# Optimization experiments

Measured on AMD Instinct MI355X. Metric: run time of the kernel, lower is better.

The kernel has to match this reference:

```python
import jax, jax.numpy as jnp
import numpy as np

LN_EPS = 1e-5
NEG_SLOPE = 0.01  # torch F.leaky_relu default


def setup_inputs() -> dict:
    key = jax.random.key(0)
    ks = jax.random.split(key, 12)
    B, N, Do, Na = 128, 32, 128, 16
    H, Dk, Dv = 4, 64, 64
    Dio = Do + Na  # 144
    g = lambda k, shape, fan_in: jax.random.normal(k, shape, jnp.float32) / np.sqrt(fan_in)
    return {
        "states": jax.random.normal(ks[0], (B, N, Do), jnp.float32),
        "policies": jax.random.uniform(ks[1], (B, N, Na), jnp.float32),
        "actions": jax.random.uniform(ks[2], (B, N, Na), jnp.float32),
        "W_se": g(ks[3], (Do, 128), Do),
        "b_se": jnp.zeros((128,), jnp.float32),
        "W_sape": g(ks[4], (Dio, 128), Dio),
        "b_sape": jnp.zeros((128,), jnp.float32),
        "Wk": g(ks[5], (H, 128, Dk), 128),
        "Wq": g(ks[6], (H, 128, Dk), 128),
        "Wv": g(ks[7], (H, 128, Dv), 128),
        "ln_g": jnp.ones((H, Dv), jnp.float32),
        "ln_b": jnp.zeros((H, Dv), jnp.float32),
        "W_f1": g(ks[8], (H * Dv, 64), H * Dv),
        "W_f2": g(ks[9], (64, 1), 64),
    }


def _layernorm(x, g, b):
    mu = x.mean(-1, keepdims=True)
    var = ((x - mu) ** 2).mean(-1, keepdims=True)
    return (x - mu) * jax.lax.rsqrt(var + LN_EPS) * g + b


def reference(states, policies, actions, W_se, b_se, W_sape, b_sape,
              Wk, Wq, Wv, ln_g, ln_b, W_f1, W_f2):
    leaky = lambda x: jax.nn.leaky_relu(x, NEG_SLOPE)
    B, N, _ = states.shape
    H, _, Dv = Wv.shape
    d_k = Wk.shape[-1]

    se = leaky(states @ W_se + b_se)  # [B,N,128]

    oa = jnp.concatenate([states, actions], axis=-1)   # [B,N,Dio]
    op = jnp.concatenate([states, policies], axis=-1)  # [B,N,Dio]
    # oap[b,j,k] = op[b,k] if j==k else oa[b,k]  (place_policies/place_actions masks)
    eye = jnp.eye(N, dtype=states.dtype)[None, :, :, None]  # [1,N,N,1]
    oap = eye * op[:, None, :, :] + (1.0 - eye) * oa[:, None, :, :]  # [B,N,N,Dio]
    x = leaky(oap @ W_sape + b_sape)  # [B,N,N,128]

    key = jnp.einsum('bnd,hde->bhne', se, Wk)  # [B,H,N,Dk]
    qry = jnp.einsum('bnd,hde->bhne', se, Wq)
    scores = jnp.einsum('bhie,bhke->bhik', qry, key) / jnp.sqrt(jnp.asarray(d_k, states.dtype))
    w = jax.nn.softmax(scores, axis=-1)  # [B,H,N,N]

    av = jnp.einsum('bjkd,hde->bhjke', x, Wv)  # [B,H,N,N,Dv]
    # node_features[b,h,i,j] = sum_k w[b,h,i,k] * av[b,h,j,k]  (fuses torch's O(N^3) repeat)
    nf = jnp.einsum('bhik,bhjke->bhije', w, av)  # [B,H,N,N,Dv]
    nf = _layernorm(nf, ln_g[None, :, None, None, :], ln_b[None, :, None, None, :])

    mh = jnp.moveaxis(nf, 1, 3).reshape(B, N, N, H * Dv)  # concat heads on last dim
    value = leaky(mh @ W_f1) @ W_f2  # [B,N,N,1]
    return value, w
```

## Files before the change

kernel.cpp:

```cpp
#include <hip/hip_runtime.h>
#include <hip/hip_bf16.h>

#define B 128
#define N 32
#define DO 128
#define NA 16
#define H 4
#define DK 64
#define DV 64
#define LN_EPS 1e-5f
#define NEG_SLOPE 0.01f

typedef unsigned short u16;
typedef __attribute__((ext_vector_type(8))) short bf16x8;
typedef __attribute__((ext_vector_type(4))) float f32x4;

__device__ __forceinline__ float leaky(float x) {
    return x >= 0.f ? x : NEG_SLOPE * x;
}

__device__ __forceinline__ u16 f2bf(float x) {
    union { float f; unsigned int u; } v; v.f = x;
    unsigned int r = (v.u + 0x7FFF + ((v.u >> 16) & 1)) >> 16;
    return (u16)r;
}

__device__ __forceinline__ float bf2f(u16 x) {
    union { unsigned int u; float f; } v; v.u = ((unsigned int)x) << 16;
    return v.f;
}

template<int CTRL>
__device__ __forceinline__ float dppadd(float x) {
    return x + __int_as_float(__builtin_amdgcn_update_dpp(
        0, __float_as_int(x), CTRL, 0xF, 0xF, true));
}

__global__ __launch_bounds__(256) void kP(
    const float* __restrict__ Wk, const float* __restrict__ Wq,
    const float* __restrict__ Wv, const float* __restrict__ W_se,
    const float* __restrict__ W_sape, const float* __restrict__ ln_g,
    const float* __restrict__ ln_b, const float* __restrict__ W_f1,
    u16* __restrict__ wTb, u16* __restrict__ wseT, u16* __restrict__ wsapeT,
    u16* __restrict__ sapeTail, u16* __restrict__ wTg,
    float* __restrict__ GW, float* __restrict__ BW)
{
    const int blk = blockIdx.x;
    const int t   = threadIdx.x;
    __shared__ float wls[8192];

    if (blk < 4) {
        const int hh = blk;
        for (int m = 0; m < 3; m++) {
            const float* src = (m == 0 ? Wq : (m == 1 ? Wk : Wv)) + hh * 8192;
            for (int idx = t; idx < 2048; idx += 256)
                ((float4*)wls)[idx] = ((const float4*)src)[idx];
            __syncthreads();
            u16* dst = wTb + (hh * 3 + m) * 8192;
            for (int idx = t; idx < 8192; idx += 256) {
                const int n = idx >> 7, k = idx & 127;
                dst[idx] = f2bf(wls[k * 64 + n]);
            }
            __syncthreads();
        }
    } else if (blk == 4 || blk == 5) {
        const float* src = (blk == 4) ? W_se : W_sape;
        u16* dst = (blk == 4) ? wseT : wsapeT;
        for (int chunk = 0; chunk < 2; chunk++) {
            const int k0 = chunk * 64;
            for (int idx = t; idx < 2048; idx += 256)
                ((float4*)wls)[idx] = ((const float4*)(src + k0 * 128))[idx];
            __syncthreads();
            for (int idx = t; idx < 8192; idx += 256) {
                const int n = idx >> 6, kk = idx & 63;
                dst[n * 128 + k0 + kk] = f2bf(wls[kk * 128 + n]);
            }
            __syncthreads();
        }
        if (blk == 5) {
            for (int idx = t; idx < 2048; idx += 256)
                wls[idx] = W_sape[128 * 128 + idx];
            __syncthreads();
            for (int idx = t; idx < 4096; idx += 256) {
                const int n = idx >> 5, kk = idx & 31;
                sapeTail[n * 32 + kk] = (kk < 16) ? f2bf(wls[kk * 128 + n]) : (u16)0;
            }
        }
    } else {
        for (int idx = t; idx < 16384; idx += 256) {
            const int hh = idx >> 12, c = (idx >> 6) & 63, ee = idx & 63;
            wTg[idx] = f2bf(ln_g[hh * 64 + ee] * W_f1[(hh * 64 + ee) * 64 + c]);
        }
        {
            const int hh = t >> 6, c = t & 63;
            float g = 0.f;
            #pragma unroll 4
            for (int ee = 0; ee < 64; ee++)
                g += ln_g[hh * 64 + ee] * W_f1[(hh * 64 + ee) * 64 + c];
            GW[t] = g;
        }
        {
            const int c = t & 63, qq = t >> 6;
            float bacc = 0.f;
            #pragma unroll 4
            for (int r = 0; r < 64; r++)
                bacc += ln_b[qq * 64 + r] * W_f1[(qq * 64 + r) * 64 + c];
            wls[qq * 64 + c] = bacc;
        }
        __syncthreads();
        if (t < 64) BW[t] = wls[t] + wls[64 + t] + wls[128 + t] + wls[192 + t];
    }
}

__global__ __launch_bounds__(1024, 8) void kB(
    const float* __restrict__ states, const float* __restrict__ actions,
    const float* __restrict__ policies,
    const float* __restrict__ b_se, const float* __restrict__ b_sape,
    const u16* __restrict__ wTb, const u16* __restrict__ wseT,
    const u16* __restrict__ wsapeT, const u16* __restrict__ sapeTail,
    const u16* __restrict__ wTg,
    float* __restrict__ w_out,
    float* __restrict__ SG, float* __restrict__ DG,
    float* __restrict__ sumS, float* __restrict__ sumS2,
    float* __restrict__ sumD, float* __restrict__ sumD2,
    float* __restrict__ dotSD)
{
    const int bh   = blockIdx.x;
    const int b    = bh >> 2;
    const int h    = bh & 3;
    const int t    = threadIdx.x;
    const int wave = t >> 6;
    const int e    = t & 63;
    const int q16  = e >> 4;
    const int l16  = e & 15;

    __shared__ alignas(16) u16   sST[32 * 136];
    __shared__ alignas(16) u16   actA[32 * 40];
    __shared__ alignas(16) u16   polA[32 * 40];
    __shared__ alignas(16) u16   sSE[32 * 136];
    __shared__ alignas(16) u16   sXA[32 * 136];
    __shared__ alignas(16) u16   sXP[32 * 136];
    __shared__ alignas(16) u16   qb[32 * 72];
    __shared__ alignas(16) u16   kb[32 * 72];
    __shared__ alignas(16) u16   avaT[64 * 40];
    __shared__ alignas(16) u16   diffb[32 * 72];
    __shared__ alignas(16) u16   wb[32 * 40];
    __shared__ alignas(16) float S32[32 * 68];
    __shared__ alignas(16) u16   Sb[32 * 72];

    const int mtP   = wave >> 3, ntP = wave & 7;
    const int bcolP = ntP * 16 + l16;
    bf16x8 pse[4];
    {
        const u16* bse_p = wseT + bcolP * 128;
        #pragma unroll
        for (int ks = 0; ks < 4; ks++)
            pse[ks] = *(const bf16x8*)&bse_p[ks * 32 + q16 * 8];
    }
    const bf16x8 btP   = *(const bf16x8*)&sapeTail[bcolP * 32 + q16 * 8];
    const float  bse_c = b_se[bcolP];
    const float  bsp_c = b_sape[bcolP];

    {
        const int r = t >> 5, c4 = (t & 31) * 4;
        const float4 s4 = *(const float4*)&states[(b * 32 + r) * 128 + c4];
        ushort4 u;
        u.x = f2bf(s4.x); u.y = f2bf(s4.y); u.z = f2bf(s4.z); u.w = f2bf(s4.w);
        *(ushort4*)&sST[r * 136 + c4] = u;
    }
    if (t < 512) {
        const int r = t >> 4, c = t & 15;
        actA[r * 40 + c]      = f2bf(actions[(b * 32 + r) * 16 + c]);
        actA[r * 40 + 16 + c] = 0;
    } else {
        const int t2 = t - 512, r = t2 >> 4, c = t2 & 15;
        polA[r * 40 + c]      = f2bf(policies[(b * 32 + r) * 16 + c]);
        polA[r * 40 + 16 + c] = 0;
    }

    bf16x8 psp[4];
    {
        const u16* bsp_p = wsapeT + bcolP * 128;
        #pragma unroll
        for (int ks = 0; ks < 4; ks++)
            psp[ks] = *(const bf16x8*)&bsp_p[ks * 32 + q16 * 8];
    }
    __syncthreads();

    f32x4 acc[2];
    bf16x8 pw0[4];
    {
        const int mt = mtP, nt = ntP;
        const int arow = mt * 16 + l16;
        const int bcol = bcolP;
        f32x4 a_se = {0.f,0.f,0.f,0.f}, a_sp = {0.f,0.f,0.f,0.f};
        f32x4 a_oa = {0.f,0.f,0.f,0.f}, a_op = {0.f,0.f,0.f,0.f};
        #pragma unroll
        for (int ks = 0; ks < 4; ks++) {
            const bf16x8 af = *(const bf16x8*)&sST[arow * 136 + ks * 32 + q16 * 8];
            a_se = __builtin_amdgcn_mfma_f32_16x16x32_bf16(af, pse[ks], a_se, 0, 0, 0);
            a_sp = __builtin_amdgcn_mfma_f32_16x16x32_bf16(af, psp[ks], a_sp, 0, 0, 0);
        }
        a_oa = __builtin_amdgcn_mfma_f32_16x16x32_bf16(
            *(const bf16x8*)&actA[arow * 40 + q16 * 8], btP, a_oa, 0, 0, 0);
        a_op = __builtin_amdgcn_mfma_f32_16x16x32_bf16(
            *(const bf16x8*)&polA[arow * 40 + q16 * 8], btP, a_op, 0, 0, 0);

        {
            const int tau0 = wave * 2;
            const int mat0 = tau0 >> 3;
            const int widx0 = (mat0 == 0) ? 0 : (mat0 == 1 ? 1 : 2);
            const int nt0 = tau0 & 3;
            const u16* wsrc0 = wTb + ((h * 3 + widx0) * 64 + nt0 * 16 + l16) * 128;
            #pragma unroll
            for (int ks = 0; ks < 4; ks++)
                pw0[ks] = *(const bf16x8*)&wsrc0[ks * 32 + q16 * 8];
        }

        const int r0 = mt * 16 + q16 * 4;
        #pragma unroll
        for (int v = 0; v < 4; v++) {
            sSE[(r0 + v) * 136 + bcol] = f2bf(leaky(a_se[v] + bse_c));
            sXA[(r0 + v) * 136 + bcol] = f2bf(leaky(a_sp[v] + a_oa[v] + bsp_c));
            sXP[(r0 + v) * 136 + bcol] = f2bf(leaky(a_sp[v] + a_op[v] + bsp_c));
        }
    }
    __syncthreads();

    #pragma unroll
    for (int p = 0; p < 2; p++) {
        const int tau = wave * 2 + p;
        const int mat = tau >> 3;
        const int mt  = (tau >> 2) & 1, nt = tau & 3;
        const u16* X  = (mat <= 1) ? sSE : (mat == 2 ? sXA : sXP);
        const int widx = (mat == 0) ? 0 : (mat == 1 ? 1 : 2);
        const int arow = mt * 16 + l16;
        const u16* wsrc = wTb + ((h * 3 + widx) * 64 + nt * 16 + l16) * 128;
        f32x4 a = {0.f, 0.f, 0.f, 0.f};
        #pragma unroll
        for (int ks = 0; ks < 4; ks++) {
            const bf16x8 af = *(const bf16x8*)&X[arow * 136 + ks * 32 + q16 * 8];
            const bf16x8 bf = (p == 0) ? pw0[ks]
                                       : *(const bf16x8*)&wsrc[ks * 32 + q16 * 8];
            a = __builtin_amdgcn_mfma_f32_16x16x32_bf16(af, bf, a, 0, 0, 0);
        }
        acc[p] = a;
    }
    #pragma unroll
    for (int p = 0; p < 2; p++) {
        const int tau = wave * 2 + p;
        const int mat = tau >> 3;
        const int mt  = (tau >> 2) & 1, nt = tau & 3;
        const int c   = nt * 16 + l16;
        const int r0  = mt * 16 + q16 * 4;
        if (mat == 0) {
            #pragma unroll
            for (int v = 0; v < 4; v++) qb[(r0 + v) * 72 + c] = f2bf(acc[p][v]);
        } else if (mat == 1) {
            #pragma unroll
            for (int v = 0; v < 4; v++) kb[(r0 + v) * 72 + c] = f2bf(acc[p][v]);
        } else if (mat == 2) {
            #pragma unroll
            for (int v = 0; v < 4; v++) avaT[c * 40 + (r0 + v)] = f2bf(acc[p][v]);
        }
    }
    __syncthreads();

    bf16x8 pwg[2];
    if (wave >= 8) {
        const int nt = (wave - 8) & 3;
        const u16* wgp = wTg + (h * 64 + nt * 16 + l16) * 64;
        #pragma unroll
        for (int ks = 0; ks < 2; ks++)
            pwg[ks] = *(const bf16x8*)&wgp[ks * 32 + q16 * 8];
    }
    if (wave < 2) {
        const int mt = wave;
        f32x4 s0 = {0.f,0.f,0.f,0.f}, s1 = {0.f,0.f,0.f,0.f};
        #pragma unroll
        for (int ks = 0; ks < 2; ks++) {
            const bf16x8 af = *(const bf16x8*)&qb[(mt * 16 + l16) * 72 + ks * 32 + q16 * 8];
            const bf16x8 b0 = *(const bf16x8*)&kb[l16 * 72 + ks * 32 + q16 * 8];
            const bf16x8 b1 = *(const bf16x8*)&kb[(16 + l16) * 72 + ks * 32 + q16 * 8];
            s0 = __builtin_amdgcn_mfma_f32_16x16x32_bf16(af, b0, s0, 0, 0, 0);
            s1 = __builtin_amdgcn_mfma_f32_16x16x32_bf16(af, b1, s1, 0, 0, 0);
        }
        #pragma unroll
        for (int v = 0; v < 4; v++) {
            float a0 = s0[v] * 0.125f, a1 = s1[v] * 0.125f;
            float mx = fmaxf(a0, a1);
            #pragma unroll
            for (int m = 1; m < 16; m <<= 1) mx = fmaxf(mx, __shfl_xor(mx, m));
            float e0 = __expf(a0 - mx), e1 = __expf(a1 - mx);
            float sm = e0 + e1;
            #pragma unroll
            for (int m = 1; m < 16; m <<= 1) sm += __shfl_xor(sm, m);
            const float inv = 1.f / sm;
            e0 *= inv; e1 *= inv;
            const int i = mt * 16 + q16 * 4 + v;
            wb[i * 40 + l16]      = f2bf(e0);
            wb[i * 40 + 16 + l16] = f2bf(e1);
            w_out[(bh * 32 + i) * 32 + l16]      = e0;
            w_out[(bh * 32 + i) * 32 + 16 + l16] = e1;
        }
    } else if (wave >= 12) {
        #pragma unroll
        for (int p = 0; p < 2; p++) {
            const int tau = wave * 2 + p;
            const int mt  = (tau >> 2) & 1, nt = tau & 3;
            const int c   = nt * 16 + l16;
            const int r0  = mt * 16 + q16 * 4;
            #pragma unroll
            for (int v = 0; v < 4; v++) {
                const float av = bf2f(avaT[c * 40 + (r0 + v)]);
                diffb[(r0 + v) * 72 + c] = f2bf(acc[p][v] - av);
            }
        }
    }
    __syncthreads();

    if (wave < 8) {
        const int mt = wave >> 2, nt = wave & 3;
        const bf16x8 af = *(const bf16x8*)&wb[(mt * 16 + l16) * 40 + q16 * 8];
        const bf16x8 bf = *(const bf16x8*)&avaT[(nt * 16 + l16) * 40 + q16 * 8];
        f32x4 a = {0.f, 0.f, 0.f, 0.f};
        a = __builtin_amdgcn_mfma_f32_16x16x32_bf16(af, bf, a, 0, 0, 0);
        const int c = nt * 16 + l16, r0 = mt * 16 + q16 * 4;
        #pragma unroll
        for (int v = 0; v < 4; v++) {
            S32[(r0 + v) * 68 + c] = a[v];
            Sb[(r0 + v) * 72 + c]  = f2bf(a[v]);
        }
    } else {
        const int w8 = wave - 8;
        const int mt = w8 >> 2, nt = w8 & 3;
        f32x4 a = {0.f, 0.f, 0.f, 0.f};
        #pragma unroll
        for (int ks = 0; ks < 2; ks++) {
            const bf16x8 af = *(const bf16x8*)&diffb[(mt * 16 + l16) * 72 + ks * 32 + q16 * 8];
            a = __builtin_amdgcn_mfma_f32_16x16x32_bf16(af, pwg[ks], a, 0, 0, 0);
        }
        const int c = nt * 16 + l16, r0 = mt * 16 + q16 * 4;
        #pragma unroll
        for (int v = 0; v < 4; v++)
            DG[(bh * 32 + r0 + v) * 64 + c] = a[v];
    }
    if (t < 32) {
        float s1 = 0.f, s2 = 0.f;
        #pragma unroll
        for (int e8 = 0; e8 < 8; e8++) {
            const uint4 u = *(const uint4*)&diffb[t * 72 + e8 * 8];
            const unsigned int uu[4] = {u.x, u.y, u.z, u.w};
            #pragma unroll
            for (int q = 0; q < 4; q++) {
                const float fl = __uint_as_float(uu[q] << 16);
                const float fh = __uint_as_float(uu[q] & 0xffff0000u);
                s1 += fl + fh;
                s2 += fl * fl + fh * fh;
            }
        }
        sumD[bh * 32 + t] = s1; sumD2[bh * 32 + t] = s2;
    }
    __syncthreads();

    if (wave < 4) {
        const int mt = wave >> 1, nt = wave & 1;
        f32x4 a = {0.f, 0.f, 0.f, 0.f};
        #pragma unroll
        for (int ks = 0; ks < 2; ks++) {
            const bf16x8 af = *(const bf16x8*)&Sb[(mt * 16 + l16) * 72 + ks * 32 + q16 * 8];
            const bf16x8 bf = *(const bf16x8*)&diffb[(nt * 16 + l16) * 72 + ks * 32 + q16 * 8];
            a = __builtin_amdgcn_mfma_f32_16x16x32_bf16(af, bf, a, 0, 0, 0);
        }
        const int j = nt * 16 + l16, r0 = mt * 16 + q16 * 4;
        #pragma unroll
        for (int v = 0; v < 4; v++)
            dotSD[(bh * 32 + r0 + v) * 32 + j] = a[v];
    } else if (wave >= 8) {
        const int w8 = wave - 8;
        const int mt = w8 >> 2, nt = w8 & 3;
        f32x4 a = {0.f, 0.f, 0.f, 0.f};
        #pragma unroll
        for (int ks = 0; ks < 2; ks++) {
            const bf16x8 af = *(const bf16x8*)&Sb[(mt * 16 + l16) * 72 + ks * 32 + q16 * 8];
            a = __builtin_amdgcn_mfma_f32_16x16x32_bf16(af, pwg[ks], a, 0, 0, 0);
        }
        const int c = nt * 16 + l16, r0 = mt * 16 + q16 * 4;
        #pragma unroll
        for (int v = 0; v < 4; v++)
            SG[(bh * 32 + r0 + v) * 64 + c] = a[v];
    } else if (t >= 256 && t < 288) {
        const int r = t - 256;
        float s1 = 0.f, s2 = 0.f;
        #pragma unroll
        for (int e4 = 0; e4 < 16; e4++) {
            const float4 v4 = *(const float4*)&S32[r * 68 + e4 * 4];
            s1 += v4.x + v4.y + v4.z + v4.w;
            s2 += v4.x * v4.x + v4.y * v4.y + v4.z * v4.z + v4.w * v4.w;
        }
        sumS[bh * 32 + r] = s1; sumS2[bh * 32 + r] = s2;
    }
}

__global__ __launch_bounds__(256) void kC(
    const float* __restrict__ SG, const float* __restrict__ DG,
    const float* __restrict__ sumS, const float* __restrict__ sumS2,
    const float* __restrict__ sumD, const float* __restrict__ sumD2,
    const float* __restrict__ dotSD, const float* __restrict__ w_all,
    const float* __restrict__ GW, const float* __restrict__ BW,
    const float* __restrict__ W_f2, float* __restrict__ value)
{
    const int blk = blockIdx.x;
    const int b   = blk >> 3;
    const int i0  = ((blk >> 1) & 3) * 8;
    const int j0  = (blk & 1) * 16;
    const int t   = threadIdx.x;
    const int w0  = t >> 6;
    const int e   = t & 63;

    __shared__ alignas(16) float pk[8 * 16 * 12];

    for (int idx = t; idx < 512; idx += 256) {
        const int ii = idx >> 6, jl = (idx >> 2) & 15, hh = idx & 3;
        const int j  = j0 + jl;
        const int hi = (b * 4 + hh) * 32 + i0 + ii;
        const int hj = (b * 4 + hh) * 32 + j;
        const float wv  = w_all[hi * 32 + j];
        const float dsd = dotSD[hi * 32 + j];
        const float mu  = (sumS[hi] + wv * sumD[hj]) * (1.f / 64.f);
        const float e2  = (sumS2[hi] + 2.f * wv * dsd + wv * wv * sumD2[hj]) * (1.f / 64.f);
        const float var = fmaxf(e2 - mu * mu, 0.f);
        const float inv = rsqrtf(var + LN_EPS);
        float* rec = &pk[(ii * 16 + jl) * 12 + hh * 3];
        rec[0] = inv;
        rec[1] = inv * wv;
        rec[2] = -inv * mu;
    }

    const float bwr = BW[e];
    const float f2v = W_f2[e];
    float gw[4], sg[8][4];
    #pragma unroll
    for (int hh = 0; hh < 4; hh++) {
        gw[hh] = GW[hh * 64 + e];
        #pragma unroll
        for (int ii = 0; ii < 8; ii++)
            sg[ii][hh] = SG[((b * 4 + hh) * 32 + i0 + ii) * 64 + e];
    }
    __syncthreads();

    for (int jb = 0; jb < 4; jb++) {
        const int jl = jb * 4 + w0;
        const int j  = j0 + jl;
        float d[4];
        #pragma unroll
        for (int hh = 0; hh < 4; hh++)
            d[hh] = DG[((b * 4 + hh) * 32 + j) * 64 + e];
        #pragma unroll
        for (int ii = 0; ii < 8; ii++) {
            const float* rec = &pk[(ii * 16 + jl) * 12];
            const f32x4 r0 = *(const f32x4*)rec;
            const f32x4 r1 = *(const f32x4*)(rec + 4);
            const f32x4 r2 = *(const f32x4*)(rec + 8);
            float z = bwr;
            z += r0[0] * sg[ii][0]; z += r0[1] * d[0]; z += r0[2] * gw[0];
            z += r0[3] * sg[ii][1]; z += r1[0] * d[1]; z += r1[1] * gw[1];
            z += r1[2] * sg[ii][2]; z += r1[3] * d[2]; z += r2[0] * gw[2];
            z += r2[1] * sg[ii][3]; z += r2[2] * d[3]; z += r2[3] * gw[3];
            float p = leaky(z) * f2v;
            p = dppadd<0x111>(p);
            p = dppadd<0x112>(p);
            p = dppadd<0x114>(p);
            p = dppadd<0x118>(p);
            p = dppadd<0x142>(p);
            p = dppadd<0x143>(p);
            if (e == 63) value[(b * 32 + i0 + ii) * 32 + j] = p;
        }
    }
}

extern "C" void kernel_launch(void* const* d_in, const int* in_sizes, int n_in,
                              void* d_out, int out_size, void* d_ws, size_t ws_size,
                              hipStream_t stream)
{
    const float* states   = (const float*)d_in[0];
    const float* policies = (const float*)d_in[1];
    const float* actions  = (const float*)d_in[2];
    const float* W_se     = (const float*)d_in[3];
    const float* b_se     = (const float*)d_in[4];
    const float* W_sape   = (const float*)d_in[5];
    const float* b_sape   = (const float*)d_in[6];
    const float* Wk       = (const float*)d_in[7];
    const float* Wq       = (const float*)d_in[8];
    const float* Wv       = (const float*)d_in[9];
    const float* ln_g     = (const float*)d_in[10];
    const float* ln_b     = (const float*)d_in[11];
    const float* W_f1     = (const float*)d_in[12];
    const float* W_f2     = (const float*)d_in[13];

    float* out_value = (float*)d_out;
    float* out_w     = out_value + B * N * N;

    float* ws    = (float*)d_ws;
    float* SG    = ws;
    float* DG    = SG    + 1048576;
    float* sumS  = DG    + 1048576;
    float* sumS2 = sumS  + 16384;
    float* sumD  = sumS2 + 16384;
    float* sumD2 = sumD  + 16384;
    float* dotSD = sumD2 + 16384;
    float* GW    = dotSD + 524288;
    float* BW    = GW    + 256;
    u16*   wTb   = (u16*)(BW + 64);
    u16*   wseT  = wTb   + 98304;
    u16*   wsapeT= wseT  + 16384;
    u16*   sapeTail = wsapeT + 16384;
    u16*   wTg   = sapeTail + 4096;

    kP<<<7, 256, 0, stream>>>(Wk, Wq, Wv, W_se, W_sape, ln_g, ln_b, W_f1,
                              wTb, wseT, wsapeT, sapeTail, wTg, GW, BW);
    kB<<<B * H, 1024, 0, stream>>>(states, actions, policies, b_se, b_sape,
                                   wTb, wseT, wsapeT, sapeTail, wTg, out_w,
                                   SG, DG, sumS, sumS2, sumD, sumD2, dotSD);
    kC<<<B * 8, 256, 0, stream>>>(SG, DG, sumS, sumS2, sumD, sumD2, dotSD,
                                  out_w, GW, BW, W_f2, out_value);
}
```

Baseline: 132.0 us.

## Fuse attention and value kernels into one per-batch block with LDS-resident intermediates

Merges the per-(batch,head) attention kernel and the value-head kernel into a single kernel with one 1024-thread block per batch. The four heads are split across wave groups. The shared state/sape embeddings are computed once per batch instead of once per head. The SG/DG projections now stay in a large shared-memory arena instead of going through global memory, and the per-pair LayerNorm coefficients are broadcast with readlane instead of a staged table. This removes a kernel launch and the global round trip of the intermediates. In exchange the grid shrinks to 128 blocks with about 143 KB of LDS each, which leaves many CUs idle and limits occupancy.

```diff
diff --git a/kernel.cpp b/kernel.cpp
--- a/kernel.cpp
+++ b/kernel.cpp
@@ -34,6 +34,10 @@
 __device__ __forceinline__ float dppadd(float x) {
     return x + __int_as_float(__builtin_amdgcn_update_dpp(
         0, __float_as_int(x), CTRL, 0xF, 0xF, true));
+}
+
+__device__ __forceinline__ float rdlane(float x, int lane) {
+    return __int_as_float(__builtin_amdgcn_readlane(__float_as_int(x), lane));
 }
 
 __global__ __launch_bounds__(256) void kP(
@@ -112,7 +116,7 @@
     }
 }
 
-__global__ __launch_bounds__(1024, 8) void kB(
+__global__ __launch_bounds__(1024, 4) void kB(
     const float* __restrict__ states, const float* __restrict__ actions,
     const float* __restrict__ policies,
     const float* __restrict__ b_se, const float* __restrict__ b_sape,
@@ -120,33 +124,39 @@
     const u16* __restrict__ wsapeT, const u16* __restrict__ sapeTail,
     const u16* __restrict__ wTg,
     float* __restrict__ w_out,
-    float* __restrict__ SG, float* __restrict__ DG,
     float* __restrict__ sumS, float* __restrict__ sumS2,
     float* __restrict__ sumD, float* __restrict__ sumD2,
-    float* __restrict__ dotSD)
+    float* __restrict__ dotSD,
+    const float* __restrict__ GW, const float* __restrict__ BW,
+    const float* __restrict__ W_f2, float* __restrict__ value)
 {
-    const int bh   = blockIdx.x;
-    const int b    = bh >> 2;
-    const int h    = bh & 3;
+    const int b    = blockIdx.x;
     const int t    = threadIdx.x;
     const int wave = t >> 6;
     const int e    = t & 63;
     const int q16  = e >> 4;
     const int l16  = e & 15;
-
-    __shared__ alignas(16) u16   sST[32 * 136];
-    __shared__ alignas(16) u16   actA[32 * 40];
-    __shared__ alignas(16) u16   polA[32 * 40];
-    __shared__ alignas(16) u16   sSE[32 * 136];
-    __shared__ alignas(16) u16   sXA[32 * 136];
-    __shared__ alignas(16) u16   sXP[32 * 136];
-    __shared__ alignas(16) u16   qb[32 * 72];
-    __shared__ alignas(16) u16   kb[32 * 72];
-    __shared__ alignas(16) u16   avaT[64 * 40];
-    __shared__ alignas(16) u16   diffb[32 * 72];
-    __shared__ alignas(16) u16   wb[32 * 40];
-    __shared__ alignas(16) float S32[32 * 68];
-    __shared__ alignas(16) u16   Sb[32 * 72];
+    const int hh   = wave >> 2;
+    const int r    = wave & 3;
+
+    __shared__ alignas(16) char sm[146432];
+    u16*   const sST  = (u16*)(sm + 0);
+    u16*   const actA = (u16*)(sm + 8704);
+    u16*   const polA = (u16*)(sm + 11264);
+    u16*   const sSE  = (u16*)(sm + 13824);
+    u16*   const sXA  = (u16*)(sm + 22528);
+    u16*   const sXP  = (u16*)(sm + 31232);
+    float* const DGf  = (float*)(sm + 0);
+    char*  const ph   = sm + 39936 + hh * 26624;
+    u16*   const qb_h    = (u16*)(ph + 0);
+    u16*   const kb_h    = (u16*)(ph + 4608);
+    float* const S32_h   = (float*)(ph + 0);
+    u16*   const diffb_h = (u16*)(ph + 9216);
+    u16*   const Sb_h    = (u16*)(ph + 13824);
+    u16*   const avaT_h  = (u16*)(ph + 18432);
+    u16*   const wb_h    = (u16*)(ph + 23552);
+    #define SGF(h)  ((float*)(sm + 39936 + (h) * 26624 + 18432))
+    #define PHH(h)  (sm + 39936 + (h) * 26624)
 
     const int mtP   = wave >> 3, ntP = wave & 7;
     const int bcolP = ntP * 16 + l16;
@@ -162,22 +172,21 @@
     const float  bsp_c = b_sape[bcolP];
 
     {
-        const int r = t >> 5, c4 = (t & 31) * 4;
-        const float4 s4 = *(const float4*)&states[(b * 32 + r) * 128 + c4];
+        const int rr = t >> 5, c4 = (t & 31) * 4;
+        const float4 s4 = *(const float4*)&states[(b * 32 + rr) * 128 + c4];
         ushort4 u;
         u.x = f2bf(s4.x); u.y = f2bf(s4.y); u.z = f2bf(s4.z); u.w = f2bf(s4.w);
-        *(ushort4*)&sST[r * 136 + c4] = u;
+        *(ushort4*)&sST[rr * 136 + c4] = u;
     }
     if (t < 512) {
-        const int r = t >> 4, c = t & 15;
-        actA[r * 40 + c]      = f2bf(actions[(b * 32 + r) * 16 + c]);
-        actA[r * 40 + 16 + c] = 0;
+        const int rr = t >> 4, c = t & 15;
+        actA[rr * 40 + c]      = f2bf(actions[(b * 32 + rr) * 16 + c]);
+        actA[rr * 40 + 16 + c] = 0;
     } else {
-        const int t2 = t - 512, r = t2 >> 4, c = t2 & 15;
-        polA[r * 40 + c]      = f2bf(policies[(b * 32 + r) * 16 + c]);
-        polA[r * 40 + 16 + c] = 0;
-    }
-
+        const int t2 = t - 512, rr = t2 >> 4, c = t2 & 15;
+        polA[rr * 40 + c]      = f2bf(policies[(b * 32 + rr) * 16 + c]);
+        polA[rr * 40 + 16 + c] = 0;
+    }
     bf16x8 psp[4];
     {
         const u16* bsp_p = wsapeT + bcolP * 128;
@@ -187,11 +196,8 @@
     }
     __syncthreads();
 
-    f32x4 acc[2];
-    bf16x8 pw0[4];
     {
-        const int mt = mtP, nt = ntP;
-        const int arow = mt * 16 + l16;
+        const int arow = mtP * 16 + l16;
         const int bcol = bcolP;
         f32x4 a_se = {0.f,0.f,0.f,0.f}, a_sp = {0.f,0.f,0.f,0.f};
         f32x4 a_oa = {0.f,0.f,0.f,0.f}, a_op = {0.f,0.f,0.f,0.f};
@@ -205,19 +211,7 @@
             *(const bf16x8*)&actA[arow * 40 + q16 * 8], btP, a_oa, 0, 0, 0);
         a_op = __builtin_amdgcn_mfma_f32_16x16x32_bf16(
             *(const bf16x8*)&polA[arow * 40 + q16 * 8], btP, a_op, 0, 0, 0);
-
-        {
-            const int tau0 = wave * 2;
-            const int mat0 = tau0 >> 3;
-            const int widx0 = (mat0 == 0) ? 0 : (mat0 == 1 ? 1 : 2);
-            const int nt0 = tau0 & 3;
-            const u16* wsrc0 = wTb + ((h * 3 + widx0) * 64 + nt0 * 16 + l16) * 128;
-            #pragma unroll
-            for (int ks = 0; ks < 4; ks++)
-                pw0[ks] = *(const bf16x8*)&wsrc0[ks * 32 + q16 * 8];
-        }
-
-        const int r0 = mt * 16 + q16 * 4;
+        const int r0 = mtP * 16 + q16 * 4;
         #pragma unroll
         for (int v = 0; v < 4; v++) {
             sSE[(r0 + v) * 136 + bcol] = f2bf(leaky(a_se[v] + bse_c));
@@ -227,61 +221,61 @@
     }
     __syncthreads();
 
-    #pragma unroll
-    for (int p = 0; p < 2; p++) {
-        const int tau = wave * 2 + p;
-        const int mat = tau >> 3;
-        const int mt  = (tau >> 2) & 1, nt = tau & 3;
-        const u16* X  = (mat <= 1) ? sSE : (mat == 2 ? sXA : sXP);
-        const int widx = (mat == 0) ? 0 : (mat == 1 ? 1 : 2);
-        const int arow = mt * 16 + l16;
-        const u16* wsrc = wTb + ((h * 3 + widx) * 64 + nt * 16 + l16) * 128;
-        f32x4 a = {0.f, 0.f, 0.f, 0.f};
-        #pragma unroll
-        for (int ks = 0; ks < 4; ks++) {
-            const bf16x8 af = *(const bf16x8*)&X[arow * 136 + ks * 32 + q16 * 8];
-            const bf16x8 bf = (p == 0) ? pw0[ks]
-                                       : *(const bf16x8*)&wsrc[ks * 32 + q16 * 8];
-            a = __builtin_amdgcn_mfma_f32_16x16x32_bf16(af, bf, a, 0, 0, 0);
-        }
-        acc[p] = a;
-    }
-    #pragma unroll
-    for (int p = 0; p < 2; p++) {
-        const int tau = wave * 2 + p;
-        const int mat = tau >> 3;
-        const int mt  = (tau >> 2) & 1, nt = tau & 3;
-        const int c   = nt * 16 + l16;
-        const int r0  = mt * 16 + q16 * 4;
-        if (mat == 0) {
-            #pragma unroll
-            for (int v = 0; v < 4; v++) qb[(r0 + v) * 72 + c] = f2bf(acc[p][v]);
-        } else if (mat == 1) {
-            #pragma unroll
-            for (int v = 0; v < 4; v++) kb[(r0 + v) * 72 + c] = f2bf(acc[p][v]);
-        } else if (mat == 2) {
-            #pragma unroll
-            for (int v = 0; v < 4; v++) avaT[c * 40 + (r0 + v)] = f2bf(acc[p][v]);
+    f32x4 acc[8];
+    {
+        const u16* X = (r <= 1) ? sSE : (r == 2 ? sXA : sXP);
+        const int widx = (r == 0) ? 0 : (r == 1 ? 1 : 2);
+        #pragma unroll
+        for (int p = 0; p < 8; p++) {
+            const int mt = p >> 2, nt = p & 3;
+            const int arow = mt * 16 + l16;
+            const u16* wsrc = wTb + ((hh * 3 + widx) * 64 + nt * 16 + l16) * 128;
+            f32x4 a = {0.f, 0.f, 0.f, 0.f};
+            #pragma unroll
+            for (int ks = 0; ks < 4; ks++) {
+                const bf16x8 af = *(const bf16x8*)&X[arow * 136 + ks * 32 + q16 * 8];
+                const bf16x8 bf = *(const bf16x8*)&wsrc[ks * 32 + q16 * 8];
+                a = __builtin_amdgcn_mfma_f32_16x16x32_bf16(af, bf, a, 0, 0, 0);
+            }
+            acc[p] = a;
+        }
+        #pragma unroll
+        for (int p = 0; p < 8; p++) {
+            const int mt = p >> 2, nt = p & 3;
+            const int c  = nt * 16 + l16;
+            const int r0 = mt * 16 + q16 * 4;
+            if (r == 0) {
+                #pragma unroll
+                for (int v = 0; v < 4; v++) qb_h[(r0 + v) * 72 + c] = f2bf(acc[p][v]);
+            } else if (r == 1) {
+                #pragma unroll
+                for (int v = 0; v < 4; v++) kb_h[(r0 + v) * 72 + c] = f2bf(acc[p][v]);
+            } else if (r == 2) {
+                #pragma unroll
+                for (int v = 0; v < 4; v++) avaT_h[c * 40 + (r0 + v)] = f2bf(acc[p][v]);
+            }
         }
     }
     __syncthreads();
 
-    bf16x8 pwg[2];
-    if (wave >= 8) {
-        const int nt = (wave - 8) & 3;
-        const u16* wgp = wTg + (h * 64 + nt * 16 + l16) * 64;
-        #pragma unroll
-        for (int ks = 0; ks < 2; ks++)
-            pwg[ks] = *(const bf16x8*)&wgp[ks * 32 + q16 * 8];
-    }
-    if (wave < 2) {
-        const int mt = wave;
+    bf16x8 pwg[4][2];
+    if (r >= 2) {
+        #pragma unroll
+        for (int nt = 0; nt < 4; nt++) {
+            const u16* wgp = wTg + (hh * 64 + nt * 16 + l16) * 64;
+            #pragma unroll
+            for (int ks = 0; ks < 2; ks++)
+                pwg[nt][ks] = *(const bf16x8*)&wgp[ks * 32 + q16 * 8];
+        }
+    }
+    if (r <= 1) {
+        const int mt = r;
         f32x4 s0 = {0.f,0.f,0.f,0.f}, s1 = {0.f,0.f,0.f,0.f};
         #pragma unroll
         for (int ks = 0; ks < 2; ks++) {
-            const bf16x8 af = *(const bf16x8*)&qb[(mt * 16 + l16) * 72 + ks * 32 + q16 * 8];
-            const bf16x8 b0 = *(const bf16x8*)&kb[l16 * 72 + ks * 32 + q16 * 8];
-            const bf16x8 b1 = *(const bf16x8*)&kb[(16 + l16) * 72 + ks * 32 + q16 * 8];
+            const bf16x8 af = *(const bf16x8*)&qb_h[(mt * 16 + l16) * 72 + ks * 32 + q16 * 8];
+            const bf16x8 b0 = *(const bf16x8*)&kb_h[l16 * 72 + ks * 32 + q16 * 8];
+            const bf16x8 b1 = *(const bf16x8*)&kb_h[(16 + l16) * 72 + ks * 32 + q16 * 8];
             s0 = __builtin_amdgcn_mfma_f32_16x16x32_bf16(af, b0, s0, 0, 0, 0);
             s1 = __builtin_amdgcn_mfma_f32_16x16x32_bf16(af, b1, s1, 0, 0, 0);
         }
@@ -292,191 +286,184 @@
             #pragma unroll
             for (int m = 1; m < 16; m <<= 1) mx = fmaxf(mx, __shfl_xor(mx, m));
             float e0 = __expf(a0 - mx), e1 = __expf(a1 - mx);
-            float sm = e0 + e1;
-            #pragma unroll
-            for (int m = 1; m < 16; m <<= 1) sm += __shfl_xor(sm, m);
-            const float inv = 1.f / sm;
+            float sm2 = e0 + e1;
+            #pragma unroll
+            for (int m = 1; m < 16; m <<= 1) sm2 += __shfl_xor(sm2, m);
+            const float inv = 1.f / sm2;
             e0 *= inv; e1 *= inv;
             const int i = mt * 16 + q16 * 4 + v;
-            wb[i * 40 + l16]      = f2bf(e0);
-            wb[i * 40 + 16 + l16] = f2bf(e1);
-            w_out[(bh * 32 + i) * 32 + l16]      = e0;
-            w_out[(bh * 32 + i) * 32 + 16 + l16] = e1;
-        }
-    } else if (wave >= 12) {
-        #pragma unroll
-        for (int p = 0; p < 2; p++) {
-            const int tau = wave * 2 + p;
-            const int mt  = (tau >> 2) & 1, nt = tau & 3;
-            const int c   = nt * 16 + l16;
-            const int r0  = mt * 16 + q16 * 4;
+            wb_h[i * 40 + l16]      = f2bf(e0);
+            wb_h[i * 40 + 16 + l16] = f2bf(e1);
+            w_out[(((b * 4 + hh) * 32) + i) * 32 + l16]      = e0;
+            w_out[(((b * 4 + hh) * 32) + i) * 32 + 16 + l16] = e1;
+        }
+    } else if (r == 3) {
+        #pragma unroll
+        for (int p = 0; p < 8; p++) {
+            const int mt = p >> 2, nt = p & 3;
+            const int c  = nt * 16 + l16;
+            const int r0 = mt * 16 + q16 * 4;
             #pragma unroll
             for (int v = 0; v < 4; v++) {
-                const float av = bf2f(avaT[c * 40 + (r0 + v)]);
-                diffb[(r0 + v) * 72 + c] = f2bf(acc[p][v] - av);
+                const float av = bf2f(avaT_h[c * 40 + (r0 + v)]);
+                diffb_h[(r0 + v) * 72 + c] = f2bf(acc[p][v] - av);
             }
         }
     }
     __syncthreads();
 
-    if (wave < 8) {
-        const int mt = wave >> 2, nt = wave & 3;
-        const bf16x8 af = *(const bf16x8*)&wb[(mt * 16 + l16) * 40 + q16 * 8];
-        const bf16x8 bf = *(const bf16x8*)&avaT[(nt * 16 + l16) * 40 + q16 * 8];
-        f32x4 a = {0.f, 0.f, 0.f, 0.f};
-        a = __builtin_amdgcn_mfma_f32_16x16x32_bf16(af, bf, a, 0, 0, 0);
-        const int c = nt * 16 + l16, r0 = mt * 16 + q16 * 4;
-        #pragma unroll
-        for (int v = 0; v < 4; v++) {
-            S32[(r0 + v) * 68 + c] = a[v];
-            Sb[(r0 + v) * 72 + c]  = f2bf(a[v]);
+    if (r <= 1) {
+        const int mt = r;
+        const bf16x8 af = *(const bf16x8*)&wb_h[(mt * 16 + l16) * 40 + q16 * 8];
+        #pragma unroll
+        for (int nt = 0; nt < 4; nt++) {
+            const bf16x8 bf = *(const bf16x8*)&avaT_h[(nt * 16 + l16) * 40 + q16 * 8];
+            f32x4 a = {0.f, 0.f, 0.f, 0.f};
+            a = __builtin_amdgcn_mfma_f32_16x16x32_bf16(af, bf, a, 0, 0, 0);
+            const int c = nt * 16 + l16, r0 = mt * 16 + q16 * 4;
+            #pragma unroll
+            for (int v = 0; v < 4; v++) {
+                S32_h[(r0 + v) * 68 + c] = a[v];
+                Sb_h[(r0 + v) * 72 + c]  = f2bf(a[v]);
+            }
         }
     } else {
-        const int w8 = wave - 8;
-        const int mt = w8 >> 2, nt = w8 & 3;
-        f32x4 a = {0.f, 0.f, 0.f, 0.f};
-        #pragma unroll
-        for (int ks = 0; ks < 2; ks++) {
-            const bf16x8 af = *(const bf16x8*)&diffb[(mt * 16 + l16) * 72 + ks * 32 + q16 * 8];
-            a = __builtin_amdgcn_mfma_f32_16x16x32_bf16(af, pwg[ks], a, 0, 0, 0);
-        }
-        const int c = nt * 16 + l16, r0 = mt * 16 + q16 * 4;
-        #pragma unroll
-        for (int v = 0; v < 4; v++)
-            DG[(bh * 32 + r0 + v) * 64 + c] = a[v];
-    }
-    if (t < 32) {
-        float s1 = 0.f, s2 = 0.f;
-        #pragma unroll
-        for (int e8 = 0; e8 < 8; e8++) {
-            const uint4 u = *(const uint4*)&diffb[t * 72 + e8 * 8];
-            const unsigned int uu[4] = {u.x, u.y, u.z, u.w};
-            #pragma unroll
-            for (int q = 0; q < 4; q++) {
-                const float fl = __uint_as_float(uu[q] << 16);
-                const float fh = __uint_as_float(uu[q] & 0xffff0000u);
-                s1 += fl + fh;
-                s2 += fl * fl + fh * fh;
-            }
-        }
-        sumD[bh * 32 + t] = s1; sumD2[bh * 32 + t] = s2;
+        const int mt = r - 2;
+        #pragma unroll
+        for (int nt = 0; nt < 4; nt++) {
+            f32x4 a = {0.f, 0.f, 0.f, 0.f};
+            #pragma unroll
+            for (int ks = 0; ks < 2; ks++) {
+                const bf16x8 af = *(const bf16x8*)&diffb_h[(mt * 16 + l16) * 72 + ks * 32 + q16 * 8];
+                a = __builtin_amdgcn_mfma_f32_16x16x32_bf16(af, pwg[nt][ks], a, 0, 0, 0);
+            }
+            const int c = nt * 16 + l16, r0 = mt * 16 + q16 * 4;
+            #pragma unroll
+            for (int v = 0; v < 4; v++)
+                DGf[hh * 2048 + (r0 + v) * 64 + c] = a[v];
+        }
     }
     __syncthreads();
 
-    if (wave < 4) {
-        const int mt = wave >> 1, nt = wave & 1;
-        f32x4 a = {0.f, 0.f, 0.f, 0.f};
-        #pragma unroll
-        for (int ks = 0; ks < 2; ks++) {
-            const bf16x8 af = *(const bf16x8*)&Sb[(mt * 16 + l16) * 72 + ks * 32 + q16 * 8];
-            const bf16x8 bf = *(const bf16x8*)&diffb[(nt * 16 + l16) * 72 + ks * 32 + q16 * 8];
-            a = __builtin_amdgcn_mfma_f32_16x16x32_bf16(af, bf, a, 0, 0, 0);
-        }
-        const int j = nt * 16 + l16, r0 = mt * 16 + q16 * 4;
-        #pragma unroll
-        for (int v = 0; v < 4; v++)
-            dotSD[(bh * 32 + r0 + v) * 32 + j] = a[v];
-    } else if (wave >= 8) {
-        const int w8 = wave - 8;
-        const int mt = w8 >> 2, nt = w8 & 3;
-        f32x4 a = {0.f, 0.f, 0.f, 0.f};
-        #pragma unroll
-        for (int ks = 0; ks < 2; ks++) {
-            const bf16x8 af = *(const bf16x8*)&Sb[(mt * 16 + l16) * 72 + ks * 32 + q16 * 8];
-            a = __builtin_amdgcn_mfma_f32_16x16x32_bf16(af, pwg[ks], a, 0, 0, 0);
-        }
-        const int c = nt * 16 + l16, r0 = mt * 16 + q16 * 4;
-        #pragma unroll
-        for (int v = 0; v < 4; v++)
-            SG[(bh * 32 + r0 + v) * 64 + c] = a[v];
-    } else if (t >= 256 && t < 288) {
-        const int r = t - 256;
-        float s1 = 0.f, s2 = 0.f;
-        #pragma unroll
-        for (int e4 = 0; e4 < 16; e4++) {
-            const float4 v4 = *(const float4*)&S32[r * 68 + e4 * 4];
-            s1 += v4.x + v4.y + v4.z + v4.w;
-            s2 += v4.x * v4.x + v4.y * v4.y + v4.z * v4.z + v4.w * v4.w;
-        }
-        sumS[bh * 32 + r] = s1; sumS2[bh * 32 + r] = s2;
-    }
-}
-
-__global__ __launch_bounds__(256) void kC(
-    const float* __restrict__ SG, const float* __restrict__ DG,
-    const float* __restrict__ sumS, const float* __restrict__ sumS2,
-    const float* __restrict__ sumD, const float* __restrict__ sumD2,
-    const float* __restrict__ dotSD, const float* __restrict__ w_all,
-    const float* __restrict__ GW, const float* __restrict__ BW,
-    const float* __restrict__ W_f2, float* __restrict__ value)
-{
-    const int blk = blockIdx.x;
-    const int b   = blk >> 3;
-    const int i0  = ((blk >> 1) & 3) * 8;
-    const int j0  = (blk & 1) * 16;
-    const int t   = threadIdx.x;
-    const int w0  = t >> 6;
-    const int e   = t & 63;
-
-    __shared__ alignas(16) float pk[8 * 16 * 12];
-
-    for (int idx = t; idx < 512; idx += 256) {
-        const int ii = idx >> 6, jl = (idx >> 2) & 15, hh = idx & 3;
-        const int j  = j0 + jl;
-        const int hi = (b * 4 + hh) * 32 + i0 + ii;
-        const int hj = (b * 4 + hh) * 32 + j;
-        const float wv  = w_all[hi * 32 + j];
-        const float dsd = dotSD[hi * 32 + j];
-        const float mu  = (sumS[hi] + wv * sumD[hj]) * (1.f / 64.f);
-        const float e2  = (sumS2[hi] + 2.f * wv * dsd + wv * wv * sumD2[hj]) * (1.f / 64.f);
-        const float var = fmaxf(e2 - mu * mu, 0.f);
-        const float inv = rsqrtf(var + LN_EPS);
-        float* rec = &pk[(ii * 16 + jl) * 12 + hh * 3];
-        rec[0] = inv;
-        rec[1] = inv * wv;
-        rec[2] = -inv * mu;
-    }
-
-    const float bwr = BW[e];
-    const float f2v = W_f2[e];
-    float gw[4], sg[8][4];
-    #pragma unroll
-    for (int hh = 0; hh < 4; hh++) {
-        gw[hh] = GW[hh * 64 + e];
-        #pragma unroll
-        for (int ii = 0; ii < 8; ii++)
-            sg[ii][hh] = SG[((b * 4 + hh) * 32 + i0 + ii) * 64 + e];
+    if (r == 0) {
+        #pragma unroll
+        for (int p = 0; p < 4; p++) {
+            const int mt = p >> 1, nt = p & 1;
+            f32x4 a = {0.f, 0.f, 0.f, 0.f};
+            #pragma unroll
+            for (int ks = 0; ks < 2; ks++) {
+                const bf16x8 af = *(const bf16x8*)&Sb_h[(mt * 16 + l16) * 72 + ks * 32 + q16 * 8];
+                const bf16x8 bf = *(const bf16x8*)&diffb_h[(nt * 16 + l16) * 72 + ks * 32 + q16 * 8];
+                a = __builtin_amdgcn_mfma_f32_16x16x32_bf16(af, bf, a, 0, 0, 0);
+            }
+            const int j = nt * 16 + l16, r0 = mt * 16 + q16 * 4;
+            #pragma unroll
+            for (int v = 0; v < 4; v++)
+                dotSD[((b * 4 + hh) * 32 + r0 + v) * 32 + j] = a[v];
+        }
+    } else if (r == 1) {
+        if (e < 32) {
+            float s1 = 0.f, s2 = 0.f;
+            #pragma unroll
+            for (int e4 = 0; e4 < 16; e4++) {
+                const float4 v4 = *(const float4*)&S32_h[e * 68 + e4 * 4];
+                s1 += v4.x + v4.y + v4.z + v4.w;
+                s2 += v4.x * v4.x + v4.y * v4.y + v4.z * v4.z + v4.w * v4.w;
+            }
+            sumS[(b * 4 + hh) * 32 + e] = s1; sumS2[(b * 4 + hh) * 32 + e] = s2;
+        } else {
+            const int rr = e - 32;
+            float s1 = 0.f, s2 = 0.f;
+            #pragma unroll
+            for (int e8 = 0; e8 < 8; e8++) {
+                const uint4 u = *(const uint4*)&diffb_h[rr * 72 + e8 * 8];
+                const unsigned int uu[4] = {u.x, u.y, u.z, u.w};
+                #pragma unroll
+                for (int q = 0; q < 4; q++) {
+                    const float fl = __uint_as_float(uu[q] << 16);
+                    const float fh = __uint_as_float(uu[q] & 0xffff0000u);
+                    s1 += fl + fh;
+                    s2 += fl * fl + fh * fh;
+                }
+            }
+            sumD[(b * 4 + hh) * 32 + rr] = s1; sumD2[(b * 4 + hh) * 32 + rr] = s2;
+        }
+    } else {
+        const int mt = r - 2;
+        #pragma unroll
+        for (int nt = 0; nt < 4; nt++) {
+            f32x4 a = {0.f, 0.f, 0.f, 0.f};
+            #pragma unroll
+            for (int ks = 0; ks < 2; ks++) {
+                const bf16x8 af = *(const bf16x8*)&Sb_h[(mt * 16 + l16) * 72 + ks * 32 + q16 * 8];
+                a = __builtin_amdgcn_mfma_f32_16x16x32_bf16(af, pwg[nt][ks], a, 0, 0, 0);
+            }
+            const int c = nt * 16 + l16, r0 = mt * 16 + q16 * 4;
+            #pragma unroll
+            for (int v = 0; v < 4; v++)
+                SGF(hh)[(r0 + v) * 64 + c] = a[v];
+        }
     }
     __syncthreads();
 
-    for (int jb = 0; jb < 4; jb++) {
-        const int jl = jb * 4 + w0;
-        const int j  = j0 + jl;
-        float d[4];
-        #pragma unroll
-        for (int hh = 0; hh < 4; hh++)
-            d[hh] = DG[((b * 4 + hh) * 32 + j) * 64 + e];
-        #pragma unroll
-        for (int ii = 0; ii < 8; ii++) {
-            const float* rec = &pk[(ii * 16 + jl) * 12];
-            const f32x4 r0 = *(const f32x4*)rec;
-            const f32x4 r1 = *(const f32x4*)(rec + 4);
-            const f32x4 r2 = *(const f32x4*)(rec + 8);
-            float z = bwr;
-            z += r0[0] * sg[ii][0]; z += r0[1] * d[0]; z += r0[2] * gw[0];
-            z += r0[3] * sg[ii][1]; z += r1[0] * d[1]; z += r1[1] * gw[1];
-            z += r1[2] * sg[ii][2]; z += r1[3] * d[2]; z += r2[0] * gw[2];
-            z += r2[1] * sg[ii][3]; z += r2[2] * d[3]; z += r2[3] * gw[3];
-            float p = leaky(z) * f2v;
-            p = dppadd<0x111>(p);
-            p = dppadd<0x112>(p);
-            p = dppadd<0x114>(p);
-            p = dppadd<0x118>(p);
-            p = dppadd<0x142>(p);
-            p = dppadd<0x143>(p);
-            if (e == 63) value[(b * 32 + i0 + ii) * 32 + j] = p;
-        }
-    }
+    {
+        const int ig = wave >> 2, w0 = wave & 3;
+        const int i0 = ig * 8;
+        const float bwr = BW[e];
+        const float f2v = W_f2[e];
+        float gw[4], sg[8][4];
+        #pragma unroll
+        for (int h4 = 0; h4 < 4; h4++) {
+            gw[h4] = GW[h4 * 64 + e];
+            #pragma unroll
+            for (int ii = 0; ii < 8; ii++)
+                sg[ii][h4] = SGF(h4)[(i0 + ii) * 64 + e];
+        }
+        const int rii  = (e & 31) >> 2;
+        const int rhh  = e & 3;
+        const int hi_r = (b * 4 + rhh) * 32 + i0 + rii;
+        const float sSr  = sumS[hi_r];
+        const float sS2r = sumS2[hi_r];
+
+        for (int jg = 0; jg < 2; jg++) {
+            for (int jb = 0; jb < 4; jb++) {
+                const int j = jg * 16 + jb * 4 + w0;
+                const int hj_r = (b * 4 + rhh) * 32 + j;
+                const float wv  = w_out[hi_r * 32 + j];
+                const float dsd = dotSD[hi_r * 32 + j];
+                const float mu  = (sSr + wv * sumD[hj_r]) * (1.f / 64.f);
+                const float e2  = (sS2r + 2.f * wv * dsd + wv * wv * sumD2[hj_r]) * (1.f / 64.f);
+                const float var = fmaxf(e2 - mu * mu, 0.f);
+                const float inv = rsqrtf(var + LN_EPS);
+                const float ra = inv, rb = inv * wv, rc = -inv * mu;
+                float d[4];
+                #pragma unroll
+                for (int h4 = 0; h4 < 4; h4++)
+                    d[h4] = DGf[h4 * 2048 + j * 64 + e];
+                #pragma unroll
+                for (int ii = 0; ii < 8; ii++) {
+                    float z = bwr;
+                    #pragma unroll
+                    for (int h4 = 0; h4 < 4; h4++) {
+                        const int lane = ii * 4 + h4;
+                        z += rdlane(ra, lane) * sg[ii][h4];
+                        z += rdlane(rb, lane) * d[h4];
+                        z += rdlane(rc, lane) * gw[h4];
+                    }
+                    float p = leaky(z) * f2v;
+                    p = dppadd<0x111>(p);
+                    p = dppadd<0x112>(p);
+                    p = dppadd<0x114>(p);
+                    p = dppadd<0x118>(p);
+                    p = dppadd<0x142>(p);
+                    p = dppadd<0x143>(p);
+                    if (e == 63) value[(b * 32 + i0 + ii) * 32 + j] = p;
+                }
+            }
+        }
+    }
+    #undef SGF
+    #undef PHH
 }
 
 extern "C" void kernel_launch(void* const* d_in, const int* in_sizes, int n_in,
@@ -519,9 +506,8 @@
 
     kP<<<7, 256, 0, stream>>>(Wk, Wq, Wv, W_se, W_sape, ln_g, ln_b, W_f1,
                               wTb, wseT, wsapeT, sapeTail, wTg, GW, BW);
-    kB<<<B * H, 1024, 0, stream>>>(states, actions, policies, b_se, b_sape,
-                                   wTb, wseT, wsapeT, sapeTail, wTg, out_w,
-                                   SG, DG, sumS, sumS2, sumD, sumD2, dotSD);
-    kC<<<B * 8, 256, 0, stream>>>(SG, DG, sumS, sumS2, sumD, sumD2, dotSD,
-                                  out_w, GW, BW, W_f2, out_value);
-}
+    kB<<<B, 1024, 0, stream>>>(states, actions, policies, b_se, b_sape,
+                               wTb, wseT, wsapeT, sapeTail, wTg, out_w,
+                               sumS, sumS2, sumD, sumD2, dotSD,
+                               GW, BW, W_f2, out_value);
+}
```

Result: slower. 142.1 us (+7.7%).
